# Performance work log

Hardware: AMD Instinct MI355X
Metric: run time of the kernel (lower is better)

Reference implementation:

```python
import jax, jax.numpy as jnp
import numpy as np

N_HEAD = 16


def setup_inputs() -> dict:
    key = jax.random.key(0)
    k1, k2, k3 = jax.random.split(key, 3)
    B, T, C = 2, 2048, 1024
    x = jax.random.normal(k1, (B, T, C), dtype=jnp.float32)
    attention_mask = jnp.zeros((B, 1, 1, T), dtype=jnp.float32)
    W_attn = jax.random.normal(k2, (C, 3 * C), dtype=jnp.float32) * 0.02
    b_attn = jnp.zeros((3 * C,), dtype=jnp.float32)
    W_proj = jax.random.normal(k3, (C, C), dtype=jnp.float32) * 0.02
    b_proj = jnp.zeros((C,), dtype=jnp.float32)
    return {"x": x, "attention_mask": attention_mask, "W_attn": W_attn,
            "b_attn": b_attn, "W_proj": W_proj, "b_proj": b_proj}


def reference(x, attention_mask, W_attn, b_attn, W_proj, b_proj):
    B, T, C = x.shape
    H = N_HEAD
    d = C // H
    qkv = x @ W_attn + b_attn                      # [B, T, 3C]
    q, k, v = jnp.split(qkv, 3, axis=-1)
    q = q.reshape(B, T, H, d).transpose(0, 2, 1, 3)  # [B, H, T, d]
    k = k.reshape(B, T, H, d).transpose(0, 2, 1, 3)
    v = v.reshape(B, T, H, d).transpose(0, 2, 1, 3)
    att = jnp.einsum('bhtd,bhsd->bhts', q, k) * (1.0 / np.sqrt(d))
    causal = jnp.tril(jnp.ones((T, T), dtype=bool))
    att = jnp.where(causal[None, None], att, jnp.float32(-10000.0))
    att = att + attention_mask                     # additive broadcast mask
    att = jax.nn.softmax(att, axis=-1)             # dropout p=0.0 -> identity
    y = jnp.einsum('bhts,bhsd->bhtd', att, v)      # [B, H, T, d]
    y = y.transpose(0, 2, 1, 3).reshape(B, T, C)
    return y @ W_proj + b_proj
```

## Files before the change

### kernel.cpp

```cpp
#include <hip/hip_runtime.h>
#include <hip/hip_bf16.h>
#include <stdint.h>

#define BATCH 2
#define TT 2048
#define CC 1024
#define NH 16
#define HD 64

typedef __attribute__((ext_vector_type(8))) short short8;
typedef __attribute__((ext_vector_type(4))) short sh4;
typedef __attribute__((ext_vector_type(4))) float f32x4;

#define MFMA16 __builtin_amdgcn_mfma_f32_16x16x32_bf16

__device__ __forceinline__ short f2bf(float f) {
  union { float f; unsigned u; } x;
  x.f = f;
  unsigned r = x.u + 0x7FFFu + ((x.u >> 16) & 1u);
  return (short)(r >> 16);
}

__device__ __forceinline__ void transpose_cast_tile(
    const float* __restrict__ W, short* __restrict__ Wt, int K, int N,
    int n0, int k0, int tid) {
  __shared__ __align__(16) float Ls[64][68];
  {
    const int r = tid >> 4, c4 = (tid & 15) * 4;
#pragma unroll
    for (int p = 0; p < 4; ++p) {
      const float4 v = *reinterpret_cast<const float4*>(
          &W[(size_t)(k0 + r + p * 16) * N + n0 + c4]);
      *reinterpret_cast<float4*>(&Ls[r + p * 16][c4]) = v;
    }
  }
  __syncthreads();
  {
    const int n = tid >> 2;
    const int kk0 = (tid & 3) * 16;
#pragma unroll
    for (int half = 0; half < 2; ++half) {
      short8 o;
#pragma unroll
      for (int t = 0; t < 8; ++t) o[t] = f2bf(Ls[kk0 + half * 8 + t][n]);
      *reinterpret_cast<short8*>(&Wt[(size_t)(n0 + n) * K + k0 + kk0 + half * 8]) = o;
    }
  }
}

__global__ __launch_bounds__(256) void prep_fused(
    const float* __restrict__ x, short* __restrict__ xb,
    const float* __restrict__ W_attn, short* __restrict__ wat,
    const float* __restrict__ W_proj, short* __restrict__ wpt) {
  const int blk = blockIdx.x;
  const int tid = threadIdx.x;
  if (blk < 2048) {
    const int i = (blk * 256 + tid) * 8;
    const float4 a = *reinterpret_cast<const float4*>(&x[i]);
    const float4 b = *reinterpret_cast<const float4*>(&x[i + 4]);
    short8 o;
    o[0] = f2bf(a.x); o[1] = f2bf(a.y); o[2] = f2bf(a.z); o[3] = f2bf(a.w);
    o[4] = f2bf(b.x); o[5] = f2bf(b.y); o[6] = f2bf(b.z); o[7] = f2bf(b.w);
    *reinterpret_cast<short8*>(&xb[i]) = o;
  } else if (blk < 2816) {
    const int b2 = blk - 2048;
    transpose_cast_tile(W_attn, wat, CC, 3 * CC, (b2 % 48) * 64,
                        (b2 / 48) * 64, tid);
  } else {
    const int b3 = blk - 2816;
    transpose_cast_tile(W_proj, wpt, CC, CC, (b3 % 16) * 64, (b3 / 16) * 64,
                        tid);
  }
}

__global__ __launch_bounds__(256) void transpose_v(
    const short* __restrict__ qkv, short* __restrict__ vT) {
  __shared__ __align__(16) short Ls[64][72];
  const int s0 = blockIdx.x * 64;
  const int bh = blockIdx.y, b = bh >> 4, h = bh & 15;
  const int tid = threadIdx.x;
  const int r = tid >> 3, c = (tid & 7) * 8;
#pragma unroll
  for (int p = 0; p < 2; ++p) {
    *reinterpret_cast<short8*>(&Ls[r + p * 32][c]) =
        *reinterpret_cast<const short8*>(
            &qkv[(size_t)(b * TT + s0 + r + p * 32) * (3 * CC) + 2 * CC +
                 h * HD + c]);
  }
  __syncthreads();
  const int d = tid >> 2, ss = (tid & 3) * 16;
  short8 o0, o1;
#pragma unroll
  for (int t = 0; t < 8; ++t) { o0[t] = Ls[ss + t][d]; o1[t] = Ls[ss + 8 + t][d]; }
  short* dst = &vT[((size_t)(bh * HD + d)) * TT + s0 + ss];
  *reinterpret_cast<short8*>(dst) = o0;
  *reinterpret_cast<short8*>(dst + 8) = o1;
}

template <bool OUT_BF16>
__global__ __launch_bounds__(256) void gemm_bt_mfma(
    const short* __restrict__ A, const short* __restrict__ Bt,
    const float* __restrict__ bias, void* __restrict__ C, int M, int N, int K,
    int QS) {
  __shared__ __align__(16) short As[2 * 128 * 32];
  __shared__ __align__(16) short Bs[2 * 128 * 32];
  const int tid = threadIdx.x;
  const int w = tid >> 6, lane = tid & 63;
  const int quad = lane >> 4, l15 = lane & 15;
  const int m0 = blockIdx.y * 128, n0 = blockIdx.x * 128;
  const int wm = (w >> 1) * 64, wn = (w & 1) * 64;

  f32x4 acc[4][4] = {};
  const int row16 = lane >> 2;
  const int c4 = (lane & 3) * 8;

  for (int k0 = 0; k0 < K; k0 += 64) {
    __syncthreads();
#pragma unroll
    for (int p = 0; p < 2; ++p) {
      const int rbase = __builtin_amdgcn_readfirstlane((w * 2 + p) * 16);
#pragma unroll
      for (int kh = 0; kh < 2; ++kh) {
        const short* ga = &A[(size_t)(m0 + rbase + row16) * K + k0 + kh * 32 + c4];
        const short* gb = &Bt[(size_t)(n0 + rbase + row16) * K + k0 + kh * 32 + c4];
        __builtin_amdgcn_global_load_lds(
            (const __attribute__((address_space(1))) void*)ga,
            (__attribute__((address_space(3))) void*)&As[kh * 4096 + rbase * 32],
            16, 0, 0);
        __builtin_amdgcn_global_load_lds(
            (const __attribute__((address_space(1))) void*)gb,
            (__attribute__((address_space(3))) void*)&Bs[kh * 4096 + rbase * 32],
            16, 0, 0);
      }
    }
    __syncthreads();

    short8 af[2][4], bfr[2][4];
#pragma unroll
    for (int kh = 0; kh < 2; ++kh) {
#pragma unroll
      for (int i = 0; i < 4; ++i)
        af[kh][i] = *reinterpret_cast<const short8*>(
            &As[kh * 4096 + (wm + i * 16 + l15) * 32 + quad * 8]);
#pragma unroll
      for (int j = 0; j < 4; ++j)
        bfr[kh][j] = *reinterpret_cast<const short8*>(
            &Bs[kh * 4096 + (wn + j * 16 + l15) * 32 + quad * 8]);
    }
#pragma unroll
    for (int kh = 0; kh < 2; ++kh)
#pragma unroll
      for (int i = 0; i < 4; ++i)
#pragma unroll
        for (int j = 0; j < 4; ++j)
          acc[i][j] = MFMA16(af[kh][i], bfr[kh][j], acc[i][j], 0, 0, 0);
  }

#pragma unroll
  for (int i = 0; i < 4; ++i) {
#pragma unroll
    for (int r = 0; r < 4; ++r) {
      const int row = m0 + wm + i * 16 + quad * 4 + r;
#pragma unroll
      for (int j = 0; j < 4; ++j) {
        const int col = n0 + wn + j * 16 + l15;
        float v = acc[i][j][r] + bias[col];
        if (col < QS) v *= 0.125f;
        if (OUT_BF16)
          ((short*)C)[(size_t)row * N + col] = f2bf(v);
        else
          ((float*)C)[(size_t)row * N + col] = v;
      }
    }
  }
}

#define PST 72
__global__ __launch_bounds__(256) void attn_mfma6(
    const short* __restrict__ qkv, const short* __restrict__ vT,
    const float* __restrict__ mask, short* __restrict__ y) {
  __shared__ __align__(16) short Ks[2][64 * PST];
  __shared__ __align__(16) short Vs[2][64 * PST];
  __shared__ __align__(16) short Ps[64 * PST];
  const int tid = threadIdx.x;
  const int w = tid >> 6, lane = tid & 63;
  const int quad = lane >> 4, l15 = lane & 15;
  const int bh = blockIdx.y, b = bh >> 4, h = bh & 15;
  const int px = blockIdx.x;
  const int qh = 31 - px;
  const int nth = qh + 1;
  const int ntot = nth + px + 1;
  const int RS = 3 * CC;

  int qt = qh;
  int qrow0 = qt * 64 + w * 16;

  short8 qf0, qf1;
  {
    const size_t qrow = (size_t)(b * TT + qrow0 + l15) * RS + h * HD + quad * 8;
    qf0 = *reinterpret_cast<const short8*>(&qkv[qrow]);
    qf1 = *reinterpret_cast<const short8*>(&qkv[qrow + 32]);
  }

  float l_run = 0.f;
  f32x4 o_acc[4] = {};

  const int sr = tid >> 3, sc = (tid & 7) * 8;
  const short* kbase = qkv + (size_t)(b * TT + sr) * RS + CC + h * HD + sc;
  const short* vbase = vT + (size_t)(bh * HD + sr) * TT + sc;
  const float* mptr = mask + b * TT + quad * 4;
  short* psrow = &Ps[(w * 16 + l15) * PST];
  const int kfo0 = quad * 8, kfo1 = 32 + quad * 8;

  short8 kpre0 = *reinterpret_cast<const short8*>(kbase);
  short8 kpre1 = *reinterpret_cast<const short8*>(kbase + (size_t)32 * RS);
  short8 vpre0 = *reinterpret_cast<const short8*>(vbase);
  short8 vpre1 = *reinterpret_cast<const short8*>(vbase + 32 * TT);

  for (int it = 0; it < ntot; ++it) {
    const int kt = (it < nth) ? it : it - nth;
    const int s0 = kt * 64;

    if (it == nth) {
#pragma unroll
      for (int r = 0; r < 4; ++r) {
        const float lr = __shfl(l_run, quad * 4 + r, 64);
        const float inv = 1.0f / lr;
        const size_t row = (size_t)(b * TT + qrow0 + quad * 4 + r);
#pragma unroll
        for (int t = 0; t < 4; ++t)
          y[row * CC + h * HD + t * 16 + l15] = f2bf(o_acc[t][r] * inv);
      }
      qt = px;
      qrow0 = qt * 64 + w * 16;
      const size_t qrow = (size_t)(b * TT + qrow0 + l15) * RS + h * HD + quad * 8;
      qf0 = *reinterpret_cast<const short8*>(&qkv[qrow]);
      qf1 = *reinterpret_cast<const short8*>(&qkv[qrow + 32]);
      l_run = 0.f;
#pragma unroll
      for (int t = 0; t < 4; ++t) o_acc[t] = f32x4{0.f, 0.f, 0.f, 0.f};
    }

    const int cur = it & 1;
    *reinterpret_cast<short8*>(&Ks[cur][sr * PST + sc]) = kpre0;
    *reinterpret_cast<short8*>(&Ks[cur][(sr + 32) * PST + sc]) = kpre1;
    *reinterpret_cast<short8*>(&Vs[cur][sr * PST + sc]) = vpre0;
    *reinterpret_cast<short8*>(&Vs[cur][(sr + 32) * PST + sc]) = vpre1;
    __syncthreads();

    if (it + 1 < ntot) {
      const int ktn = (it + 1 == nth) ? 0 : kt + 1;
      const short* kp = kbase + (size_t)ktn * 64 * RS;
      const short* vp = vbase + ktn * 64;
      kpre0 = *reinterpret_cast<const short8*>(kp);
      kpre1 = *reinterpret_cast<const short8*>(kp + (size_t)32 * RS);
      vpre0 = *reinterpret_cast<const short8*>(vp);
      vpre1 = *reinterpret_cast<const short8*>(vp + 32 * TT);
    }

    f32x4 sa[4] = {};
#pragma unroll
    for (int j = 0; j < 4; ++j) {
      const short8 kf0 = *reinterpret_cast<const short8*>(
          &Ks[cur][(j * 16 + l15) * PST + kfo0]);
      const short8 kf1 = *reinterpret_cast<const short8*>(
          &Ks[cur][(j * 16 + l15) * PST + kfo1]);
      sa[j] = MFMA16(kf0, qf0, sa[j], 0, 0, 0);
      sa[j] = MFMA16(kf1, qf1, sa[j], 0, 0, 0);
    }

    f32x4 mv[4];
#pragma unroll
    for (int j = 0; j < 4; ++j)
      mv[j] = *reinterpret_cast<const f32x4*>(&mptr[s0 + j * 16]);

    float rs = 0.f;
    const bool boundary = (kt == qt);
    const int qg = qrow0 + l15;
#pragma unroll
    for (int j = 0; j < 4; ++j) {
      sh4 pw;
#pragma unroll
      for (int r = 0; r < 4; ++r) {
        float v = sa[j][r] + mv[j][r];
        if (boundary) {
          const int sg = s0 + j * 16 + quad * 4 + r;
          if (sg > qg) v = -10000.0f;
        }
        const float p = __expf(v);
        union { float f; unsigned u; } pu;
        pu.f = p;
        pw[r] = (short)(pu.u >> 16);
        pu.u &= 0xffff0000u;
        rs += pu.f;
      }
      *reinterpret_cast<sh4*>(&psrow[j * 16 + quad * 4]) = pw;
    }
    rs += __shfl_xor(rs, 16, 64);
    rs += __shfl_xor(rs, 32, 64);
    l_run += rs;

    const short8 pf0 = *reinterpret_cast<const short8*>(&psrow[kfo0]);
    const short8 pf1 = *reinterpret_cast<const short8*>(&psrow[kfo1]);
#pragma unroll
    for (int t = 0; t < 4; ++t) {
      const short8 vf0 = *reinterpret_cast<const short8*>(
          &Vs[cur][(t * 16 + l15) * PST + kfo0]);
      const short8 vf1 = *reinterpret_cast<const short8*>(
          &Vs[cur][(t * 16 + l15) * PST + kfo1]);
      o_acc[t] = MFMA16(pf0, vf0, o_acc[t], 0, 0, 0);
      o_acc[t] = MFMA16(pf1, vf1, o_acc[t], 0, 0, 0);
    }
  }

#pragma unroll
  for (int r = 0; r < 4; ++r) {
    const float lr = __shfl(l_run, quad * 4 + r, 64);
    const float inv = 1.0f / lr;
    const size_t row = (size_t)(b * TT + qrow0 + quad * 4 + r);
#pragma unroll
    for (int t = 0; t < 4; ++t)
      y[row * CC + h * HD + t * 16 + l15] = f2bf(o_acc[t][r] * inv);
  }
}

extern "C" void kernel_launch(void* const* d_in, const int* in_sizes, int n_in,
                              void* d_out, int out_size, void* d_ws,
                              size_t ws_size, hipStream_t stream) {
  const float* x = (const float*)d_in[0];
  const float* attn_mask = (const float*)d_in[1];
  const float* W_attn = (const float*)d_in[2];
  const float* b_attn = (const float*)d_in[3];
  const float* W_proj = (const float*)d_in[4];
  const float* b_proj = (const float*)d_in[5];
  float* out = (float*)d_out;

  const int M = BATCH * TT;

  short* xb = (short*)d_ws;
  short* wat = xb + (size_t)M * CC;
  short* wpt = wat + (size_t)(3 * CC) * CC;
  short* qkvb = wpt + (size_t)CC * CC;
  short* yb = qkvb + (size_t)M * 3 * CC;
  short* vTb = yb + (size_t)M * CC;

  prep_fused<<<3072, 256, 0, stream>>>(x, xb, W_attn, wat, W_proj, wpt);

  gemm_bt_mfma<true><<<dim3((3 * CC) / 128, M / 128), 256, 0, stream>>>(
      xb, wat, b_attn, qkvb, M, 3 * CC, CC, CC);

  transpose_v<<<dim3(TT / 64, BATCH * NH), 256, 0, stream>>>(qkvb, vTb);

  attn_mfma6<<<dim3(16, BATCH * NH), 256, 0, stream>>>(
      qkvb, vTb, attn_mask, yb);

  gemm_bt_mfma<false><<<dim3(CC / 128, M / 128), 256, 0, stream>>>(
      yb, wpt, b_proj, out, M, CC, CC, 0);
}
```

Before: 207.4 us.

## Enlarge attention query tile to 128 rows with two subtiles per wave

```diff
diff --git a/kernel.cpp b/kernel.cpp
--- a/kernel.cpp
+++ b/kernel.cpp
@@ -175,41 +175,43 @@
   }
 }
 
-#define PST 72
-__global__ __launch_bounds__(256) void attn_mfma6(
+#define PST 70
+__global__ __launch_bounds__(256) void attn_mfma7(
     const short* __restrict__ qkv, const short* __restrict__ vT,
     const float* __restrict__ mask, short* __restrict__ y) {
   __shared__ __align__(16) short Ks[2][64 * PST];
   __shared__ __align__(16) short Vs[2][64 * PST];
-  __shared__ __align__(16) short Ps[64 * PST];
+  __shared__ __align__(16) short Ps[128 * PST];
   const int tid = threadIdx.x;
   const int w = tid >> 6, lane = tid & 63;
   const int quad = lane >> 4, l15 = lane & 15;
-  const int bh = blockIdx.y, b = bh >> 4, h = bh & 15;
-  const int px = blockIdx.x;
-  const int qh = 31 - px;
-  const int nth = qh + 1;
-  const int ntot = nth + px + 1;
+  const int n = blockIdx.x;
+  const int bh = (n & 7) | (((n >> 3) & 3) << 3);
+  const int px = n >> 5;
+  const int b = bh >> 4, h = bh & 15;
+  const int qh = 15 - px;
+  const int nth = 2 * qh + 2;
+  const int ntot = 34;
   const int RS = 3 * CC;
 
   int qt = qh;
-  int qrow0 = qt * 64 + w * 16;
-
-  short8 qf0, qf1;
-  {
-    const size_t qrow = (size_t)(b * TT + qrow0 + l15) * RS + h * HD + quad * 8;
-    qf0 = *reinterpret_cast<const short8*>(&qkv[qrow]);
-    qf1 = *reinterpret_cast<const short8*>(&qkv[qrow + 32]);
-  }
-
-  float l_run = 0.f;
-  f32x4 o_acc[4] = {};
+  int qb = qt * 128 + w * 32;
+
+  short8 qf[2][2];
+#pragma unroll
+  for (int st = 0; st < 2; ++st) {
+    const size_t qrow = (size_t)(b * TT + qb + st * 16 + l15) * RS + h * HD + quad * 8;
+    qf[st][0] = *reinterpret_cast<const short8*>(&qkv[qrow]);
+    qf[st][1] = *reinterpret_cast<const short8*>(&qkv[qrow + 32]);
+  }
+
+  float l_run[2] = {0.f, 0.f};
+  f32x4 o_acc[2][4] = {};
 
   const int sr = tid >> 3, sc = (tid & 7) * 8;
   const short* kbase = qkv + (size_t)(b * TT + sr) * RS + CC + h * HD + sc;
   const short* vbase = vT + (size_t)(bh * HD + sr) * TT + sc;
   const float* mptr = mask + b * TT + quad * 4;
-  short* psrow = &Ps[(w * 16 + l15) * PST];
   const int kfo0 = quad * 8, kfo1 = 32 + quad * 8;
 
   short8 kpre0 = *reinterpret_cast<const short8*>(kbase);
@@ -223,22 +225,28 @@
 
     if (it == nth) {
 #pragma unroll
-      for (int r = 0; r < 4; ++r) {
-        const float lr = __shfl(l_run, quad * 4 + r, 64);
-        const float inv = 1.0f / lr;
-        const size_t row = (size_t)(b * TT + qrow0 + quad * 4 + r);
-#pragma unroll
-        for (int t = 0; t < 4; ++t)
-          y[row * CC + h * HD + t * 16 + l15] = f2bf(o_acc[t][r] * inv);
+      for (int st = 0; st < 2; ++st) {
+#pragma unroll
+        for (int r = 0; r < 4; ++r) {
+          const float lr = __shfl(l_run[st], quad * 4 + r, 64);
+          const float inv = 1.0f / lr;
+          const size_t row = (size_t)(b * TT + qb + st * 16 + quad * 4 + r);
+#pragma unroll
+          for (int t = 0; t < 4; ++t)
+            y[row * CC + h * HD + t * 16 + l15] = f2bf(o_acc[st][t][r] * inv);
+        }
       }
       qt = px;
-      qrow0 = qt * 64 + w * 16;
-      const size_t qrow = (size_t)(b * TT + qrow0 + l15) * RS + h * HD + quad * 8;
-      qf0 = *reinterpret_cast<const short8*>(&qkv[qrow]);
-      qf1 = *reinterpret_cast<const short8*>(&qkv[qrow + 32]);
-      l_run = 0.f;
-#pragma unroll
-      for (int t = 0; t < 4; ++t) o_acc[t] = f32x4{0.f, 0.f, 0.f, 0.f};
+      qb = qt * 128 + w * 32;
+#pragma unroll
+      for (int st = 0; st < 2; ++st) {
+        const size_t qrow = (size_t)(b * TT + qb + st * 16 + l15) * RS + h * HD + quad * 8;
+        qf[st][0] = *reinterpret_cast<const short8*>(&qkv[qrow]);
+        qf[st][1] = *reinterpret_cast<const short8*>(&qkv[qrow + 32]);
+        l_run[st] = 0.f;
+#pragma unroll
+        for (int t = 0; t < 4; ++t) o_acc[st][t] = f32x4{0.f, 0.f, 0.f, 0.f};
+      }
     }
 
     const int cur = it & 1;
@@ -258,15 +266,23 @@
       vpre1 = *reinterpret_cast<const short8*>(vp + 32 * TT);
     }
 
-    f32x4 sa[4] = {};
+    const bool act0 = (s0 <= qb + 15);
+    const bool act1 = (s0 <= qb + 31);
+    if (!act1) continue;
+
+    f32x4 sa[2][4] = {};
 #pragma unroll
     for (int j = 0; j < 4; ++j) {
       const short8 kf0 = *reinterpret_cast<const short8*>(
           &Ks[cur][(j * 16 + l15) * PST + kfo0]);
       const short8 kf1 = *reinterpret_cast<const short8*>(
           &Ks[cur][(j * 16 + l15) * PST + kfo1]);
-      sa[j] = MFMA16(kf0, qf0, sa[j], 0, 0, 0);
-      sa[j] = MFMA16(kf1, qf1, sa[j], 0, 0, 0);
+      if (act0) {
+        sa[0][j] = MFMA16(kf0, qf[0][0], sa[0][j], 0, 0, 0);
+        sa[0][j] = MFMA16(kf1, qf[0][1], sa[0][j], 0, 0, 0);
+      }
+      sa[1][j] = MFMA16(kf0, qf[1][0], sa[1][j], 0, 0, 0);
+      sa[1][j] = MFMA16(kf1, qf[1][1], sa[1][j], 0, 0, 0);
     }
 
     f32x4 mv[4];
@@ -274,53 +290,72 @@
     for (int j = 0; j < 4; ++j)
       mv[j] = *reinterpret_cast<const f32x4*>(&mptr[s0 + j * 16]);
 
-    float rs = 0.f;
-    const bool boundary = (kt == qt);
-    const int qg = qrow0 + l15;
-#pragma unroll
-    for (int j = 0; j < 4; ++j) {
-      sh4 pw;
-#pragma unroll
-      for (int r = 0; r < 4; ++r) {
-        float v = sa[j][r] + mv[j][r];
-        if (boundary) {
-          const int sg = s0 + j * 16 + quad * 4 + r;
-          if (sg > qg) v = -10000.0f;
+#pragma unroll
+    for (int st = 0; st < 2; ++st) {
+      if (st == 0 && !act0) continue;
+      const int qs = qb + st * 16;
+      short* psrow = &Ps[(w * 32 + st * 16 + l15) * PST];
+      float rs = 0.f;
+      const bool boundary = (s0 + 63 > qs);
+      const int qg = qs + l15;
+#pragma unroll
+      for (int j = 0; j < 4; ++j) {
+        sh4 pw;
+#pragma unroll
+        for (int r = 0; r < 4; ++r) {
+          float v = sa[st][j][r] + mv[j][r];
+          if (boundary) {
+            const int sg = s0 + j * 16 + quad * 4 + r;
+            if (sg > qg) v = -10000.0f;
+          }
+          const float p = __expf(v);
+          union { float f; unsigned u; } pu;
+          pu.f = p;
+          pw[r] = (short)(pu.u >> 16);
+          pu.u &= 0xffff0000u;
+          rs += pu.f;
         }
-        const float p = __expf(v);
-        union { float f; unsigned u; } pu;
-        pu.f = p;
-        pw[r] = (short)(pu.u >> 16);
-        pu.u &= 0xffff0000u;
-        rs += pu.f;
-      }
-      *reinterpret_cast<sh4*>(&psrow[j * 16 + quad * 4]) = pw;
-    }
-    rs += __shfl_xor(rs, 16, 64);
-    rs += __shfl_xor(rs, 32, 64);
-    l_run += rs;
-
-    const short8 pf0 = *reinterpret_cast<const short8*>(&psrow[kfo0]);
-    const short8 pf1 = *reinterpret_cast<const short8*>(&psrow[kfo1]);
+        *reinterpret_cast<sh4*>(&psrow[j * 16 + quad * 4]) = pw;
+      }
+      rs += __shfl_xor(rs, 16, 64);
+      rs += __shfl_xor(rs, 32, 64);
+      l_run[st] += rs;
+    }
+
+    short8 pf[2][2];
+#pragma unroll
+    for (int st = 0; st < 2; ++st) {
+      if (st == 0 && !act0) continue;
+      short* psrow = &Ps[(w * 32 + st * 16 + l15) * PST];
+      pf[st][0] = *reinterpret_cast<const short8*>(&psrow[kfo0]);
+      pf[st][1] = *reinterpret_cast<const short8*>(&psrow[kfo1]);
+    }
 #pragma unroll
     for (int t = 0; t < 4; ++t) {
       const short8 vf0 = *reinterpret_cast<const short8*>(
           &Vs[cur][(t * 16 + l15) * PST + kfo0]);
       const short8 vf1 = *reinterpret_cast<const short8*>(
           &Vs[cur][(t * 16 + l15) * PST + kfo1]);
-      o_acc[t] = MFMA16(pf0, vf0, o_acc[t], 0, 0, 0);
-      o_acc[t] = MFMA16(pf1, vf1, o_acc[t], 0, 0, 0);
-    }
-  }
-
-#pragma unroll
-  for (int r = 0; r < 4; ++r) {
-    const float lr = __shfl(l_run, quad * 4 + r, 64);
-    const float inv = 1.0f / lr;
-    const size_t row = (size_t)(b * TT + qrow0 + quad * 4 + r);
-#pragma unroll
-    for (int t = 0; t < 4; ++t)
-      y[row * CC + h * HD + t * 16 + l15] = f2bf(o_acc[t][r] * inv);
+      if (act0) {
+        o_acc[0][t] = MFMA16(pf[0][0], vf0, o_acc[0][t], 0, 0, 0);
+        o_acc[0][t] = MFMA16(pf[0][1], vf1, o_acc[0][t], 0, 0, 0);
+      }
+      o_acc[1][t] = MFMA16(pf[1][0], vf0, o_acc[1][t], 0, 0, 0);
+      o_acc[1][t] = MFMA16(pf[1][1], vf1, o_acc[1][t], 0, 0, 0);
+    }
+  }
+
+#pragma unroll
+  for (int st = 0; st < 2; ++st) {
+#pragma unroll
+    for (int r = 0; r < 4; ++r) {
+      const float lr = __shfl(l_run[st], quad * 4 + r, 64);
+      const float inv = 1.0f / lr;
+      const size_t row = (size_t)(b * TT + qb + st * 16 + quad * 4 + r);
+#pragma unroll
+      for (int t = 0; t < 4; ++t)
+        y[row * CC + h * HD + t * 16 + l15] = f2bf(o_acc[st][t][r] * inv);
+    }
   }
 }
 
@@ -351,8 +386,7 @@
 
   transpose_v<<<dim3(TT / 64, BATCH * NH), 256, 0, stream>>>(qkvb, vTb);
 
-  attn_mfma6<<<dim3(16, BATCH * NH), 256, 0, stream>>>(
-      qkvb, vTb, attn_mask, yb);
+  attn_mfma7<<<256, 256, 0, stream>>>(qkvb, vTb, attn_mask, yb);
 
   gemm_bt_mfma<false><<<dim3(CC / 128, M / 128), 256, 0, stream>>>(
       yb, wpt, b_proj, out, M, CC, CC, 0);
```

New measurement: 260.0 us. 25.4% more time.
